# Optimization experiments

Hardware: AMD Instinct MI355X
Metric: run time of the kernel (lower is better)

Reference implementation:

```python
import jax, jax.numpy as jnp
import numpy as np

D = 1024
H = 16
HD = D // H  # 64
HIDDEN = ((int(D * 8 / 3) + 63) // 64) * 64  # 2752
EPS = 1e-6


def rmsnorm(x, w):
    rms = jnp.sqrt(jnp.mean(x * x, axis=-1, keepdims=True) + EPS)
    return x / rms * w


def setup_inputs() -> dict:
    key = jax.random.key(0)
    ks = jax.random.split(key, 12)
    s = lambda fan_in: 1.0 / np.sqrt(fan_in)
    return {
        "x": jax.random.normal(ks[0], (4, 16, 256, D), dtype=jnp.float32),
        "time_emb": jax.random.normal(ks[1], (4, D), dtype=jnp.float32),
        "norm1_w": jnp.ones((D,), dtype=jnp.float32),
        "norm2_w": jnp.ones((D,), dtype=jnp.float32),
        # weights stored (in, out), i.e. transpose of torch nn.Linear.weight
        "qkv_w": jax.random.normal(ks[2], (D, 3 * H * HD), dtype=jnp.float32) * s(D),
        "out_w": jax.random.normal(ks[3], (H * HD, D), dtype=jnp.float32) * s(H * HD),
        "w1": jax.random.normal(ks[4], (D, HIDDEN), dtype=jnp.float32) * s(D),
        "w2": jax.random.normal(ks[5], (D, HIDDEN), dtype=jnp.float32) * s(D),
        "w3": jax.random.normal(ks[6], (HIDDEN, D), dtype=jnp.float32) * s(HIDDEN),
        "mod_w": jax.random.normal(ks[7], (D, 6 * D), dtype=jnp.float32) * s(D),
        "mod_b": jnp.zeros((6 * D,), dtype=jnp.float32),
    }


def spatial_attention(h, qkv_w, out_w):
    # h: (B, T, S, D); attention over S independently per (B, T)
    B, T, S, _ = h.shape
    qkv = jnp.einsum('btsd,de->btse', h, qkv_w)  # (B,T,S,3*H*HD)
    qkv = qkv.reshape(B, T, S, 3, H, HD)
    q, k, v = qkv[..., 0, :, :], qkv[..., 1, :, :], qkv[..., 2, :, :]  # (B,T,S,H,HD)
    scale = HD ** -0.5
    scores = jnp.einsum('btqhd,btkhd->bthqk', q, k) * scale  # (B,T,H,S,S)
    attn = jax.nn.softmax(scores, axis=-1)
    out = jnp.einsum('bthqk,btkhd->btqhd', attn, v).reshape(B, T, S, H * HD)
    return jnp.einsum('btse,ed->btsd', out, out_w)


def reference(x, time_emb, norm1_w, norm2_w, qkv_w, out_w, w1, w2, w3, mod_w, mod_b):
    # adaLN modulation from (B, D) time_emb -> broadcast over (T, S)
    mod = jax.nn.silu(time_emb) @ mod_w + mod_b  # (B, 6D)
    mod = mod[:, None, None, :]  # (B,1,1,6D)
    shift1, scale1, gate1, shift2, scale2, gate2 = jnp.split(mod, 6, axis=-1)

    h = rmsnorm(x, norm1_w) * (1.0 + scale1) + shift1
    h = spatial_attention(h, qkv_w, out_w)
    x = x + gate1 * h

    h = rmsnorm(x, norm2_w) * (1.0 + scale2) + shift2
    h = (jax.nn.silu(h @ w1) * (h @ w2)) @ w3  # SwiGLU
    x = x + gate2 * h
    return x
```

## Files before the change

kernel.cpp:

```cpp
#include <hip/hip_runtime.h>
#include <stdint.h>


using bf16x8 = __attribute__((ext_vector_type(8))) short;
using f32x4  = __attribute__((ext_vector_type(4))) float;

typedef __attribute__((address_space(3))) uint16_t lds16_t;

__device__ __forceinline__ float bf2f(uint16_t h) {
  union { uint32_t u; float f; } v; v.u = ((uint32_t)h) << 16; return v.f;
}
__device__ __forceinline__ uint16_t f2bf(float f) {
  union { float f; uint32_t u; } v; v.f = f;
  uint32_t r = v.u + 0x7FFFu + ((v.u >> 16) & 1u);
  return (uint16_t)(r >> 16);
}
__device__ __forceinline__ float silu(float x) { return x / (1.0f + __expf(-x)); }

__device__ __forceinline__ void gload16(const uint16_t* g, lds16_t* l) {
  __builtin_amdgcn_global_load_lds(
      (const __attribute__((address_space(1))) void*)g,
      (__attribute__((address_space(3))) void*)l, 16, 0, 0);
}

__global__ __launch_bounds__(256)
void transpose_cast(const float* __restrict__ w, uint16_t* __restrict__ wt,
                    int K, int N, int ldt) {
  __shared__ float tile[32][33];
  int n0 = blockIdx.x * 32, k0 = blockIdx.y * 32;
  int tx = threadIdx.x & 31, ty = threadIdx.x >> 5;
#pragma unroll
  for (int it = 0; it < 4; ++it) {
    int r = ty + it * 8;
    tile[r][tx] = w[(size_t)(k0 + r) * N + n0 + tx];
  }
  __syncthreads();
#pragma unroll
  for (int it = 0; it < 4; ++it) {
    int r = ty + it * 8;
    wt[(size_t)(n0 + r) * ldt + k0 + tx] = f2bf(tile[tx][r]);
  }
}

__global__ __launch_bounds__(1024)
void mod_kernel(const float* __restrict__ te, const float* __restrict__ mw,
                const float* __restrict__ mb, float* __restrict__ mod) {
  __shared__ float ste[4096];
  __shared__ float red[4][4][256];
  int tid = threadIdx.x;
  for (int i = tid; i < 4096; i += 1024) { float v = te[i]; ste[i] = silu(v); }
  __syncthreads();
  int kslice = tid >> 8, cl = tid & 255;
  int col = blockIdx.x * 256 + cl;
  float acc[4] = {0.f, 0.f, 0.f, 0.f};
  for (int kk = 0; kk < 256; ++kk) {
    int k = kslice * 256 + kk;
    float wv = mw[k * 6144 + col];
#pragma unroll
    for (int b = 0; b < 4; ++b) acc[b] += ste[b * 1024 + k] * wv;
  }
#pragma unroll
  for (int b = 0; b < 4; ++b) red[kslice][b][cl] = acc[b];
  __syncthreads();
  if (kslice == 0) {
#pragma unroll
    for (int b = 0; b < 4; ++b)
      mod[b * 6144 + col] =
          red[0][b][cl] + red[1][b][cl] + red[2][b][cl] + red[3][b][cl] + mb[col];
  }
}

__global__ __launch_bounds__(256)
void norm_kernel(const float* __restrict__ xf,
                 const float* __restrict__ w, const float* __restrict__ mod,
                 int shift_off, int scale_off, uint16_t* __restrict__ out) {
  int row = blockIdx.x;
  int b = row >> 12;
  int tid = threadIdx.x;
  float4 t = *(const float4*)(xf + (size_t)row * 1024 + tid * 4);
  float v[4] = {t.x, t.y, t.z, t.w};
  float ss = v[0] * v[0] + v[1] * v[1] + v[2] * v[2] + v[3] * v[3];
#pragma unroll
  for (int off = 1; off < 64; off <<= 1) ss += __shfl_xor(ss, off);
  __shared__ float red[4];
  if ((tid & 63) == 0) red[tid >> 6] = ss;
  __syncthreads();
  float tot = red[0] + red[1] + red[2] + red[3];
  float rinv = rsqrtf(tot * (1.0f / 1024.0f) + 1e-6f);
  const float* mrow = mod + b * 6144;
  uint16_t o[4];
#pragma unroll
  for (int c = 0; c < 4; ++c) {
    int col = tid * 4 + c;
    float hv = v[c] * rinv * w[col] * (1.0f + mrow[scale_off + col]) + mrow[shift_off + col];
    o[c] = f2bf(hv);
  }
  uint2 pk;
  pk.x = (uint32_t)o[0] | ((uint32_t)o[1] << 16);
  pk.y = (uint32_t)o[2] | ((uint32_t)o[3] << 16);
  *(uint2*)(out + (size_t)row * 1024 + tid * 4) = pk;
}


#define BAR __builtin_amdgcn_s_barrier()
#define LGKM0                                            \
  do {                                                   \
    asm volatile("s_waitcnt lgkmcnt(0)" ::: "memory");   \
    __builtin_amdgcn_sched_barrier(0);                   \
  } while (0)
#define VMW(N) asm volatile("s_waitcnt vmcnt(" #N ")" ::: "memory")

#define GRD4(DST, BASE, ROWB, SWZ)                                           \
  {                                                                          \
    _Pragma("unroll") for (int q_ = 0; q_ < 4; ++q_)                         \
        DST[q_] = *(const bf16x8*)((BASE) + ((ROWB) + q_ * 16 + col) * 64 +  \
                                   (SWZ));                                   \
  }

#define MM16(I0, AF)                                                         \
  {                                                                          \
    __builtin_amdgcn_s_setprio(1);                                           \
    _Pragma("unroll") for (int q_ = 0; q_ < 4; ++q_) {                       \
      _Pragma("unroll") for (int j_ = 0; j_ < 4; ++j_)                       \
          acc[(I0) + q_][j_] = __builtin_amdgcn_mfma_f32_16x16x32_bf16(      \
              AF[q_], bf[j_], acc[(I0) + q_][j_], 0, 0, 0);                  \
    }                                                                        \
    __builtin_amdgcn_s_setprio(0);                                           \
  }

#define ADST(S, H, G) ((lds16_t*)As[(S)] + (H) * 8192 + (G) * 4096 + sdoff)
#define BDST(S, H, G) ((lds16_t*)Bs[(S)] + (H) * 8192 + (G) * 4096 + sdoff)

#define TILE(S, KA, KB, DO_A, DO_B, VMTAIL)                                  \
  {                                                                          \
    bf16x8 af[4], bf[4];                                                     \
                                                                \
    GRD4(af, As[S], wm * 128, swz0);                                         \
    GRD4(bf, Bs[S], wn * 64, swz0);                                          \
    if (DO_A) {                                                              \
      gload16(aS00 + (KA), ADST((S) ^ 1, 0, 0));                             \
      gload16(aS01 + (KA), ADST((S) ^ 1, 0, 1));                             \
    }                                                                        \
    BAR; LGKM0;                                                              \
    MM16(0, af);                                                             \
    BAR;                                                                     \
                                                                \
    GRD4(af, As[S], wm * 128 + 64, swz0);                                    \
    if (DO_A) {                                                              \
      gload16(aS10 + (KA), ADST((S) ^ 1, 1, 0));                             \
      gload16(aS11 + (KA), ADST((S) ^ 1, 1, 1));                             \
    }                                                                        \
    BAR; LGKM0;                                                              \
    MM16(4, af);                                                             \
    BAR;                                                                     \
                                                                \
    GRD4(af, As[S], wm * 128, swz1);                                         \
    GRD4(bf, Bs[S], wn * 64, swz1);                                          \
    BAR; LGKM0;                                                              \
    MM16(0, af);                                                             \
    BAR;                                                                     \
                                                                \
    GRD4(af, As[S], wm * 128 + 64, swz1);                                    \
    if (DO_B) {                                                              \
      gload16(bS00 + (KB), BDST(S, 0, 0));                                   \
      gload16(bS01 + (KB), BDST(S, 0, 1));                                   \
      gload16(bS10 + (KB), BDST(S, 1, 0));                                   \
      gload16(bS11 + (KB), BDST(S, 1, 1));                                   \
    }                                                                        \
    BAR; LGKM0;                                                              \
    MM16(4, af);                                                             \
    VMTAIL;                                                                  \
    BAR;                                                                     \
  }

template <int MODE>
__global__ __launch_bounds__(512)
void gemm256(const uint16_t* __restrict__ A, int lda,
             const uint16_t* __restrict__ Bt, int ldb,
             int N, int K, int ldc,
             uint16_t* __restrict__ obf, const float* __restrict__ xin,
             const float* __restrict__ mod, const uint16_t* __restrict__ h1,
             float* __restrict__ xio) {
  __shared__ uint16_t As[2][16384];
  __shared__ uint16_t Bs[2][16384];
  const int tiles_n = N >> 8;
  const int xcd = blockIdx.x & 7;
  const int bslot = blockIdx.x >> 3;
  const int tm = (bslot / tiles_n) * 8 + xcd;
  const int tn = bslot % tiles_n;
  const int m0 = tm * 256, n0 = tn * 256;
  const int tid = threadIdx.x;
  const int wave = tid >> 6, lane = tid & 63;
  const int wm = wave >> 2, wn = wave & 3;
  const int col = lane & 15, quad = lane >> 4;
  const int c7 = col & 7;
  const int swz0 = (quad ^ c7) << 3;
  const int swz1 = ((4 + quad) ^ c7) << 3;
  const int sdoff = wave * 512 + lane * 8;

  const int srl = lane >> 3;
  const int sl8 = ((lane & 7) ^ srl) << 3;
  const int rg0 = wave * 8 + srl;
  const int rg1 = 64 + wave * 8 + srl;
  const uint16_t* aS00 = A + (size_t)(m0 + rg0) * lda + sl8;
  const uint16_t* aS01 = A + (size_t)(m0 + rg1) * lda + sl8;
  const uint16_t* aS10 = A + (size_t)(m0 + 128 + rg0) * lda + sl8;
  const uint16_t* aS11 = A + (size_t)(m0 + 128 + rg1) * lda + sl8;
  const uint16_t* bS00 = Bt + (size_t)(n0 + rg0) * ldb + sl8;
  const uint16_t* bS01 = Bt + (size_t)(n0 + rg1) * ldb + sl8;
  const uint16_t* bS10 = Bt + (size_t)(n0 + 128 + rg0) * ldb + sl8;
  const uint16_t* bS11 = Bt + (size_t)(n0 + 128 + rg1) * ldb + sl8;

  f32x4 acc[8][4];
#pragma unroll
  for (int i = 0; i < 8; ++i)
#pragma unroll
    for (int j = 0; j < 4; ++j) acc[i][j] = (f32x4){0.f, 0.f, 0.f, 0.f};

  gload16(bS00, BDST(0, 0, 0)); gload16(bS01, BDST(0, 0, 1));
  gload16(bS10, BDST(0, 1, 0)); gload16(bS11, BDST(0, 1, 1));
  gload16(aS00, ADST(0, 0, 0)); gload16(aS01, ADST(0, 0, 1));
  gload16(aS10, ADST(0, 1, 0)); gload16(aS11, ADST(0, 1, 1));
  gload16(bS00 + 64, BDST(1, 0, 0)); gload16(bS01 + 64, BDST(1, 0, 1));
  gload16(bS10 + 64, BDST(1, 1, 0)); gload16(bS11 + 64, BDST(1, 1, 1));
  VMW(4);
  BAR;

  const int NT = K >> 6;
  int k0 = 0;
  for (int t = 0; t + 2 < NT; t += 2) {
    TILE(0, k0 + 64, k0 + 128, true, true, VMW(4));
    TILE(1, k0 + 128, k0 + 192, true, true, VMW(4));
    k0 += 128;
  }
  TILE(0, k0 + 64, 0, true, false, VMW(0));
  TILE(1, 0, 0, false, false, (void)0);

#pragma unroll
  for (int i = 0; i < 8; ++i) {
#pragma unroll
    for (int j = 0; j < 4; ++j) {
#pragma unroll
      for (int r = 0; r < 4; ++r) {
        int row = m0 + wm * 128 + i * 16 + quad * 4 + r;
        int cn = n0 + wn * 64 + j * 16 + col;
        float c = acc[i][j][r];
        if (MODE == 0) {
          obf[(size_t)row * ldc + cn] = f2bf(c);
        } else if (MODE == 1) {
          int b = row >> 12;
          size_t idx = (size_t)row * 1024 + cn;
          float g = mod[b * 6144 + 2048 + cn];
          xio[idx] = xin[idx] + g * c;
        } else if (MODE == 2) {
          obf[(size_t)row * ldc + cn] = f2bf(silu(c));
        } else if (MODE == 3) {
          size_t idx = (size_t)row * ldc + cn;
          obf[idx] = f2bf(bf2f(h1[idx]) * c);
        } else {
          int b = row >> 12;
          size_t idx = (size_t)row * 1024 + cn;
          float g = mod[b * 6144 + 5120 + cn];
          xio[idx] = xio[idx] + g * c;
        }
      }
    }
  }
}

__global__ __launch_bounds__(256)
void attn_kernel(const uint16_t* __restrict__ qkv, uint16_t* __restrict__ out) {
  __shared__ uint16_t lds[32768];
  const int tid = threadIdx.x;
  const int bid = blockIdx.x;
  const int slice = bid >> 2, qc = bid & 3;
  const int bt = slice >> 4, h = slice & 15;
  const int row0 = bt * 256;
  const int wave = tid >> 6, lane = tid & 63;
  const int col = lane & 15, quad = lane >> 4;

  {
    int kr = tid;
    const uint16_t* kp = qkv + (size_t)(row0 + kr) * 3072 + 1024 + h * 64;
    uint16_t* ks = lds + kr * 64;
#pragma unroll
    for (int kc = 0; kc < 8; ++kc) {
      uint4 v = *(const uint4*)(kp + kc * 8);
      *(uint4*)(ks + ((kc ^ (kr & 7)) << 3)) = v;
    }
  }
  {
    int p = tid & 127, dh = tid >> 7;
    const uint16_t* vp0 = qkv + (size_t)(row0 + 2 * p) * 3072 + 2048 + h * 64 + dh * 32;
    const uint16_t* vp1 = vp0 + 3072;
    uint16_t r0[32], r1[32];
#pragma unroll
    for (int i = 0; i < 4; ++i) {
      *(uint4*)(r0 + i * 8) = *(const uint4*)(vp0 + i * 8);
      *(uint4*)(r1 + i * 8) = *(const uint4*)(vp1 + i * 8);
    }
    uint32_t* vt = (uint32_t*)(lds + 16384);
    int krc = p >> 2;
#pragma unroll
    for (int i = 0; i < 32; ++i) {
      int d = dh * 32 + i;
      uint32_t val = (uint32_t)r0[i] | ((uint32_t)r1[i] << 16);
      vt[d * 128 + ((krc ^ (d & 7)) << 2) + (p & 3)] = val;
    }
  }
  __syncthreads();

  const int qrow = qc * 64 + wave * 16 + col;
  const uint16_t* qp = qkv + (size_t)(row0 + qrow) * 3072 + h * 64;
  bf16x8 aq0 = *(const bf16x8*)(qp + quad * 8);
  bf16x8 aq1 = *(const bf16x8*)(qp + 32 + quad * 8);

  f32x4 sc[16];
#pragma unroll
  for (int t = 0; t < 16; ++t) {
    int n = t * 16 + col;
    const uint16_t* kb = lds + n * 64;
    bf16x8 b0 = *(const bf16x8*)(kb + ((quad ^ (n & 7)) << 3));
    bf16x8 b1 = *(const bf16x8*)(kb + (((4 + quad) ^ (n & 7)) << 3));
    f32x4 s = (f32x4){0.f, 0.f, 0.f, 0.f};
    s = __builtin_amdgcn_mfma_f32_16x16x32_bf16(aq0, b0, s, 0, 0, 0);
    s = __builtin_amdgcn_mfma_f32_16x16x32_bf16(aq1, b1, s, 0, 0, 0);
    sc[t] = s;
  }

  const float scale = 0.125f;
  float inv[4];
#pragma unroll
  for (int i = 0; i < 4; ++i) {
    float m = -1e30f;
#pragma unroll
    for (int t = 0; t < 16; ++t) m = fmaxf(m, sc[t][i]);
    m = fmaxf(m, __shfl_xor(m, 1));
    m = fmaxf(m, __shfl_xor(m, 2));
    m = fmaxf(m, __shfl_xor(m, 4));
    m = fmaxf(m, __shfl_xor(m, 8));
    m *= scale;
    float sum = 0.f;
#pragma unroll
    for (int t = 0; t < 16; ++t) {
      float p = __expf(sc[t][i] * scale - m);
      sc[t][i] = p;
      sum += p;
    }
    sum += __shfl_xor(sum, 1);
    sum += __shfl_xor(sum, 2);
    sum += __shfl_xor(sum, 4);
    sum += __shfl_xor(sum, 8);
    inv[i] = 1.0f / sum;
  }
  __syncthreads();

  uint16_t* P = lds + wave * 4096;
#pragma unroll
  for (int t = 0; t < 16; ++t) {
    int pcb = t * 2 + (col >> 3);
#pragma unroll
    for (int i = 0; i < 4; ++i) {
      int r = quad * 4 + i;
      P[r * 256 + ((pcb ^ (r & 7)) << 3) + (col & 7)] = f2bf(sc[t][i] * inv[i]);
    }
  }

  f32x4 o[4];
#pragma unroll
  for (int nt = 0; nt < 4; ++nt) o[nt] = (f32x4){0.f, 0.f, 0.f, 0.f};
  const uint16_t* Vt = lds + 16384;
#pragma unroll
  for (int c = 0; c < 8; ++c) {
    int pc = c * 4 + quad;
    bf16x8 ap = *(const bf16x8*)(P + col * 256 + ((pc ^ (col & 7)) << 3));
#pragma unroll
    for (int nt = 0; nt < 4; ++nt) {
      int d = nt * 16 + col;
      bf16x8 bv = *(const bf16x8*)(Vt + d * 256 + ((pc ^ (d & 7)) << 3));
      o[nt] = __builtin_amdgcn_mfma_f32_16x16x32_bf16(ap, bv, o[nt], 0, 0, 0);
    }
  }

#pragma unroll
  for (int nt = 0; nt < 4; ++nt) {
#pragma unroll
    for (int r = 0; r < 4; ++r) {
      int grow = row0 + qc * 64 + wave * 16 + quad * 4 + r;
      int gcol = h * 64 + nt * 16 + col;
      out[(size_t)grow * 1024 + gcol] = f2bf(o[nt][r]);
    }
  }
}

extern "C" void kernel_launch(void* const* d_in, const int* in_sizes, int n_in,
                              void* d_out, int out_size, void* d_ws, size_t ws_size,
                              hipStream_t stream) {
  const float* x        = (const float*)d_in[0];
  const float* time_emb = (const float*)d_in[1];
  const float* norm1_w  = (const float*)d_in[2];
  const float* norm2_w  = (const float*)d_in[3];
  const float* qkv_w    = (const float*)d_in[4];
  const float* out_w    = (const float*)d_in[5];
  const float* w1       = (const float*)d_in[6];
  const float* w2       = (const float*)d_in[7];
  const float* w3       = (const float*)d_in[8];
  const float* mod_w    = (const float*)d_in[9];
  const float* mod_b    = (const float*)d_in[10];
  float* out = (float*)d_out;

  char* ws = (char*)d_ws;
  float*    mod    = (float*)(ws);
  uint16_t* wqkv_t = (uint16_t*)(ws + 98304);
  uint16_t* wout_t = (uint16_t*)(ws + 6389760);
  uint16_t* w1t    = (uint16_t*)(ws + 8486912);
  uint16_t* w2t    = (uint16_t*)(ws + 14254080);
  uint16_t* w3t    = (uint16_t*)(ws + 20021248);
  uint16_t* hbuf   = (uint16_t*)(ws + 25788416);
  uint16_t* qkvb   = (uint16_t*)(ws + 59342848);
  uint16_t* hid    = qkvb;

  hipMemsetAsync(w1t, 0, (size_t)2816 * 1024 * 2, stream);
  hipMemsetAsync(w2t, 0, (size_t)2816 * 1024 * 2, stream);
  hipMemsetAsync(w3t, 0, (size_t)1024 * 2816 * 2, stream);

  dim3 blk(256);
  transpose_cast<<<dim3(96, 32), blk, 0, stream>>>(qkv_w, wqkv_t, 1024, 3072, 1024);
  transpose_cast<<<dim3(32, 32), blk, 0, stream>>>(out_w, wout_t, 1024, 1024, 1024);
  transpose_cast<<<dim3(86, 32), blk, 0, stream>>>(w1, w1t, 1024, 2752, 1024);
  transpose_cast<<<dim3(86, 32), blk, 0, stream>>>(w2, w2t, 1024, 2752, 1024);
  transpose_cast<<<dim3(32, 86), blk, 0, stream>>>(w3, w3t, 2752, 1024, 2816);

  mod_kernel<<<24, 1024, 0, stream>>>(time_emb, mod_w, mod_b, mod);

  norm_kernel<<<16384, blk, 0, stream>>>(x, norm1_w, mod, 0, 1024, hbuf);

  gemm256<0><<<768, 512, 0, stream>>>(hbuf, 1024, wqkv_t, 1024, 3072, 1024, 3072,
                                      qkvb, nullptr, nullptr, nullptr, nullptr);
  attn_kernel<<<4096, blk, 0, stream>>>(qkvb, hbuf);

  gemm256<1><<<256, 512, 0, stream>>>(hbuf, 1024, wout_t, 1024, 1024, 1024, 1024,
                                      nullptr, x, mod, nullptr, out);
  norm_kernel<<<16384, blk, 0, stream>>>(out, norm2_w, mod, 3072, 4096, hbuf);

  gemm256<2><<<704, 512, 0, stream>>>(hbuf, 1024, w1t, 1024, 2816, 1024, 2816,
                                      hid, nullptr, nullptr, nullptr, nullptr);
  gemm256<3><<<704, 512, 0, stream>>>(hbuf, 1024, w2t, 1024, 2816, 1024, 2816,
                                      hid, nullptr, nullptr, hid, nullptr);
  gemm256<4><<<256, 512, 0, stream>>>(hid, 2816, w3t, 2816, 1024, 2816, 1024,
                                      nullptr, nullptr, mod, nullptr, out);
}
```

Baseline: 861.9 us.

## Fuse SwiGLU gate and up GEMMs into one dual-accumulator kernel

Replaces the two separate w1 and w2 GEMM launches with a single kernel that loads each A tile once and multiplies it against both B1 and B2 tiles, keeping two accumulator sets and writing silu(c1)*c2 in the epilogue. This removes the intermediate write and re-read of the hidden buffer and the second read of the normalized activations. The tile shrinks to 256x128 with 1408 blocks, and register pressure rises from holding two accumulators. LDS fragment reads are also switched to inline-asm ds_read_b128, and a sched_barrier is added before the epilogue.

Result: faster. 757.6 us (-12.1%).

```diff
diff --git a/kernel.cpp b/kernel.cpp
--- a/kernel.cpp
+++ b/kernel.cpp
@@ -21,6 +21,13 @@
   __builtin_amdgcn_global_load_lds(
       (const __attribute__((address_space(1))) void*)g,
       (__attribute__((address_space(3))) void*)l, 16, 0, 0);
+}
+
+__device__ __forceinline__ bf16x8 lds_rd_b128(const uint16_t* p) {
+  bf16x8 r;
+  uint32_t a = (uint32_t)(uintptr_t)(const lds16_t*)p;
+  asm volatile("ds_read_b128 %0, %1" : "=v"(r) : "v"(a) : "memory");
+  return r;
 }
 
 __global__ __launch_bounds__(256)
@@ -101,7 +108,6 @@
   *(uint2*)(out + (size_t)row * 1024 + tid * 4) = pk;
 }
 
-
 #define BAR __builtin_amdgcn_s_barrier()
 #define LGKM0                                            \
   do {                                                   \
@@ -113,8 +119,8 @@
 #define GRD4(DST, BASE, ROWB, SWZ)                                           \
   {                                                                          \
     _Pragma("unroll") for (int q_ = 0; q_ < 4; ++q_)                         \
-        DST[q_] = *(const bf16x8*)((BASE) + ((ROWB) + q_ * 16 + col) * 64 +  \
-                                   (SWZ));                                   \
+        DST[q_] = lds_rd_b128((BASE) + ((ROWB) + q_ * 16 + col) * 64 +       \
+                              (SWZ));                                        \
   }
 
 #define MM16(I0, AF)                                                         \
@@ -236,6 +242,8 @@
   TILE(0, k0 + 64, 0, true, false, VMW(0));
   TILE(1, 0, 0, false, false, (void)0);
 
+  __builtin_amdgcn_sched_barrier(0);
+
 #pragma unroll
   for (int i = 0; i < 8; ++i) {
 #pragma unroll
@@ -252,17 +260,149 @@
           size_t idx = (size_t)row * 1024 + cn;
           float g = mod[b * 6144 + 2048 + cn];
           xio[idx] = xin[idx] + g * c;
-        } else if (MODE == 2) {
-          obf[(size_t)row * ldc + cn] = f2bf(silu(c));
-        } else if (MODE == 3) {
-          size_t idx = (size_t)row * ldc + cn;
-          obf[idx] = f2bf(bf2f(h1[idx]) * c);
         } else {
           int b = row >> 12;
           size_t idx = (size_t)row * 1024 + cn;
           float g = mod[b * 6144 + 5120 + cn];
           xio[idx] = xio[idx] + g * c;
         }
+      }
+    }
+  }
+}
+
+#define MMF(ACC, AF, BF)                                                     \
+  {                                                                          \
+    __builtin_amdgcn_s_setprio(1);                                           \
+    _Pragma("unroll") for (int i_ = 0; i_ < 4; ++i_) {                       \
+      _Pragma("unroll") for (int j_ = 0; j_ < 4; ++j_)                       \
+          ACC[i_][j_] = __builtin_amdgcn_mfma_f32_16x16x32_bf16(             \
+              AF[i_], BF[j_], ACC[i_][j_], 0, 0, 0);                         \
+    }                                                                        \
+    __builtin_amdgcn_s_setprio(0);                                           \
+  }
+
+#define FAD(S, H)  ((lds16_t*)As[(S)]  + (H) * 4096 + sdoff)
+#define FB1D(S, H) ((lds16_t*)B1s[(S)] + (H) * 4096 + sdoff)
+#define FB2D(S, H) ((lds16_t*)B2s[(S)] + (H) * 4096 + sdoff)
+
+#define FTILE(S, KN, KB, DO_AB2, DO_B1, VMTAIL)                              \
+  {                                                                          \
+    bf16x8 af[4], bb[4];                                                     \
+                      \
+    GRD4(af, As[S], wm * 64, swz0);                                          \
+    GRD4(bb, B1s[S], wn * 64, swz0);                                         \
+    if (DO_AB2) {                                                            \
+      gload16(aS[0] + (KN), FAD((S) ^ 1, 0));                                \
+      gload16(aS[1] + (KN), FAD((S) ^ 1, 1));                                \
+      gload16(b2S[0] + (KN), FB2D((S) ^ 1, 0));                              \
+      gload16(b2S[1] + (KN), FB2D((S) ^ 1, 1));                              \
+    }                                                                        \
+    BAR; LGKM0;                                                              \
+    MMF(acc1, af, bb);                                                       \
+    BAR;                                                                     \
+                                        \
+    GRD4(bb, B2s[S], wn * 64, swz0);                                         \
+    if (DO_AB2) {                                                            \
+      gload16(aS[2] + (KN), FAD((S) ^ 1, 2));                                \
+      gload16(aS[3] + (KN), FAD((S) ^ 1, 3));                                \
+    }                                                                        \
+    BAR; LGKM0;                                                              \
+    MMF(acc2, af, bb);                                                       \
+    BAR;                                                                     \
+                                                     \
+    GRD4(af, As[S], wm * 64, swz1);                                          \
+    GRD4(bb, B1s[S], wn * 64, swz1);                                         \
+    BAR; LGKM0;                                                              \
+    MMF(acc1, af, bb);                                                       \
+    BAR;                                                                     \
+                                             \
+    GRD4(bb, B2s[S], wn * 64, swz1);                                         \
+    if (DO_B1) {                                                             \
+      gload16(b1S[0] + (KB), FB1D(S, 0));                                    \
+      gload16(b1S[1] + (KB), FB1D(S, 1));                                    \
+    }                                                                        \
+    BAR; LGKM0;                                                              \
+    MMF(acc2, af, bb);                                                       \
+    VMTAIL;                                                                  \
+    BAR;                                                                     \
+  }
+
+__global__ __launch_bounds__(512)
+void gemm_ffn(const uint16_t* __restrict__ A, const uint16_t* __restrict__ B1t,
+              const uint16_t* __restrict__ B2t, uint16_t* __restrict__ outp) {
+  __shared__ uint16_t As[2][16384];
+  __shared__ uint16_t B1s[2][8192];
+  __shared__ uint16_t B2s[2][8192];
+  const int lda = 1024, ldb = 1024, ldc = 2816;
+  const int tiles_n = 22;
+  const int xcd = blockIdx.x & 7;
+  const int bslot = blockIdx.x >> 3;
+  const int tm = (bslot / tiles_n) * 8 + xcd;
+  const int tn = bslot % tiles_n;
+  const int m0 = tm * 256, n0 = tn * 128;
+  const int tid = threadIdx.x;
+  const int wave = tid >> 6, lane = tid & 63;
+  const int wm = wave >> 1, wn = wave & 1;
+  const int col = lane & 15, quad = lane >> 4;
+  const int c7 = col & 7;
+  const int swz0 = (quad ^ c7) << 3;
+  const int swz1 = ((4 + quad) ^ c7) << 3;
+  const int sdoff = wave * 512 + lane * 8;
+  const int srl = lane >> 3;
+  const int sl8 = ((lane & 7) ^ srl) << 3;
+  const int rg = wave * 8 + srl;
+
+  const uint16_t* aS[4];
+#pragma unroll
+  for (int h = 0; h < 4; ++h)
+    aS[h] = A + (size_t)(m0 + h * 64 + rg) * lda + sl8;
+  const uint16_t* b1S[2]; const uint16_t* b2S[2];
+#pragma unroll
+  for (int h = 0; h < 2; ++h) {
+    b1S[h] = B1t + (size_t)(n0 + h * 64 + rg) * ldb + sl8;
+    b2S[h] = B2t + (size_t)(n0 + h * 64 + rg) * ldb + sl8;
+  }
+
+  f32x4 acc1[4][4], acc2[4][4];
+#pragma unroll
+  for (int i = 0; i < 4; ++i)
+#pragma unroll
+    for (int j = 0; j < 4; ++j) {
+      acc1[i][j] = (f32x4){0.f, 0.f, 0.f, 0.f};
+      acc2[i][j] = (f32x4){0.f, 0.f, 0.f, 0.f};
+    }
+
+#pragma unroll
+  for (int h = 0; h < 4; ++h) gload16(aS[h], FAD(0, h));
+  gload16(b1S[0], FB1D(0, 0)); gload16(b1S[1], FB1D(0, 1));
+  gload16(b2S[0], FB2D(0, 0)); gload16(b2S[1], FB2D(0, 1));
+  gload16(b1S[0] + 64, FB1D(1, 0)); gload16(b1S[1] + 64, FB1D(1, 1));
+  VMW(2);
+  BAR;
+
+  int k0 = 0;
+  for (int t = 0; t + 2 < 16; t += 2) {
+    FTILE(0, k0 + 64, k0 + 128, true, true, VMW(2));
+    FTILE(1, k0 + 128, k0 + 192, true, true, VMW(2));
+    k0 += 128;
+  }
+  FTILE(0, k0 + 64, 0, true, false, VMW(0));
+  FTILE(1, 0, 0, false, false, (void)0);
+
+  __builtin_amdgcn_sched_barrier(0);
+
+#pragma unroll
+  for (int i = 0; i < 4; ++i) {
+#pragma unroll
+    for (int j = 0; j < 4; ++j) {
+#pragma unroll
+      for (int r = 0; r < 4; ++r) {
+        int row = m0 + wm * 64 + i * 16 + quad * 4 + r;
+        int cn = n0 + wn * 64 + j * 16 + col;
+        float c1 = acc1[i][j][r];
+        float c2 = acc2[i][j][r];
+        outp[(size_t)row * ldc + cn] = f2bf(silu(c1) * c2);
       }
     }
   }
@@ -443,10 +583,8 @@
                                       nullptr, x, mod, nullptr, out);
   norm_kernel<<<16384, blk, 0, stream>>>(out, norm2_w, mod, 3072, 4096, hbuf);
 
-  gemm256<2><<<704, 512, 0, stream>>>(hbuf, 1024, w1t, 1024, 2816, 1024, 2816,
-                                      hid, nullptr, nullptr, nullptr, nullptr);
-  gemm256<3><<<704, 512, 0, stream>>>(hbuf, 1024, w2t, 1024, 2816, 1024, 2816,
-                                      hid, nullptr, nullptr, hid, nullptr);
+  gemm_ffn<<<1408, 512, 0, stream>>>(hbuf, w1t, w2t, hid);
+
   gemm256<4><<<256, 512, 0, stream>>>(hid, 2816, w3t, 2816, 1024, 2816, 1024,
                                       nullptr, nullptr, mod, nullptr, out);
 }
```
